# Optimization experiments

Hardware: AMD Instinct MI355X
Metric: run time of the kernel (lower is better)

Reference implementation:

```python
import jax, jax.numpy as jnp
import numpy as np

DIM = 2048
N_HEADS = 16
Q_LORA = 1536
KV_LORA = 512
NOPE = 128
ROPE = 64
V_DIM = 128
B, T = 1, 3072
EPS = 1e-6


def rmsnorm(x, w):
    var = jnp.mean(jnp.square(x), axis=-1, keepdims=True)
    return x * jax.lax.rsqrt(var + EPS) * w


def apply_rope(x, cos, sin):
    # x: (B, T, H, d); cos/sin: (T, d//2) -> broadcast (1, T, 1, d//2)
    c = cos[None, :, None, :]
    s = sin[None, :, None, :]
    x1 = x[..., 0::2]
    x2 = x[..., 1::2]
    r1 = x1 * c - x2 * s
    r2 = x1 * s + x2 * c
    return jnp.stack([r1, r2], axis=-1).reshape(x.shape)


def setup_inputs() -> dict:
    key = jax.random.key(0)
    ks = jax.random.split(key, 10)
    std = 0.02
    x = jax.random.normal(ks[0], (B, T, DIM), dtype=jnp.float32)
    # RoPE angles: position * inv_freq, shape (T, ROPE//2)
    inv_freq = 1.0 / (10000.0 ** (np.arange(0, ROPE, 2, dtype=np.float32) / ROPE))
    freqs = jnp.asarray(np.arange(T, dtype=np.float32)[:, None] * inv_freq[None, :])
    # additive causal mask (T, T)
    mask = jnp.where(jnp.tril(jnp.ones((T, T), dtype=bool)), 0.0, -jnp.inf).astype(jnp.float32)
    wq_down = jax.random.normal(ks[1], (DIM, Q_LORA), dtype=jnp.float32) * std
    q_norm_w = jnp.ones((Q_LORA,), dtype=jnp.float32)
    wq_nope = jax.random.normal(ks[2], (Q_LORA, N_HEADS * NOPE), dtype=jnp.float32) * std
    wq_rope = jax.random.normal(ks[3], (Q_LORA, N_HEADS * ROPE), dtype=jnp.float32) * std
    wkv_down = jax.random.normal(ks[4], (DIM, KV_LORA + ROPE), dtype=jnp.float32) * std
    kv_norm_w = jnp.ones((KV_LORA,), dtype=jnp.float32)
    wkv_up = jax.random.normal(ks[5], (KV_LORA, N_HEADS * (NOPE + V_DIM)), dtype=jnp.float32) * std
    wo = jax.random.normal(ks[6], (N_HEADS * V_DIM, DIM), dtype=jnp.float32) * std
    return {
        'x': x, 'freqs': freqs, 'mask': mask,
        'wq_down': wq_down, 'q_norm_w': q_norm_w, 'wq_nope': wq_nope,
        'wq_rope': wq_rope, 'wkv_down': wkv_down, 'kv_norm_w': kv_norm_w,
        'wkv_up': wkv_up, 'wo': wo,
    }


def reference(x, freqs, mask, wq_down, q_norm_w, wq_nope, wq_rope,
              wkv_down, kv_norm_w, wkv_up, wo):
    cos, sin = jnp.cos(freqs), jnp.sin(freqs)
    # Q path: down-project, RMSNorm, split nope/rope heads
    q_lat = rmsnorm(x @ wq_down, q_norm_w)                      # (B,T,Q_LORA)
    q_nope = (q_lat @ wq_nope).reshape(B, T, N_HEADS, NOPE)
    q_rope = apply_rope((q_lat @ wq_rope).reshape(B, T, N_HEADS, ROPE), cos, sin)
    q = jnp.concatenate([q_nope, q_rope], axis=-1)              # (B,T,H,192)
    # KV path: joint down-projection -> latent c_kv + raw rope key
    kvd = x @ wkv_down                                          # (B,T,KV_LORA+ROPE)
    c_kv = kvd[..., :KV_LORA]
    k_rope_raw = kvd[..., KV_LORA:]                             # (B,T,ROPE)
    k_rope = jnp.broadcast_to(k_rope_raw[:, :, None, :], (B, T, N_HEADS, ROPE))
    k_rope = apply_rope(k_rope, cos, sin)
    kv_up = (rmsnorm(c_kv, kv_norm_w) @ wkv_up).reshape(B, T, N_HEADS, NOPE + V_DIM)
    k_nope = kv_up[..., :NOPE]
    v = kv_up[..., NOPE:]                                       # (B,T,H,V_DIM)
    k = jnp.concatenate([k_nope, k_rope], axis=-1)              # (B,T,H,192)
    scale = (NOPE + ROPE) ** (-0.5)
    attn = jnp.einsum('bqhd,bkhd->bhqk', q, k) * scale + mask[None, None]
    attn = jax.nn.softmax(attn, axis=-1)                        # dropout p=0 (eval)
    out = jnp.einsum('bhqk,bkhd->bqhd', attn, v).reshape(B, T, N_HEADS * V_DIM)
    return out @ wo                                             # (B,T,DIM)
```

## Files before the change

### kernel.cpp

```cpp
#include <hip/hip_runtime.h>
#include <hip/hip_bf16.h>

typedef __bf16 bf16_t;
typedef __bf16 bf16x8 __attribute__((ext_vector_type(8)));
typedef float f32x4 __attribute__((ext_vector_type(4)));

#define T_SEQ 3072
#define DIM 2048
#define NH 16
#define QLORA 1536
#define KVLORA 512
#define NOPE 128
#define ROPE 64
#define VDIM 128
#define HD 192
#define SCALE 0.07216878364870323f
#define CHUNK 12

#define T1KV_LD 2112
#define QNR_LD 3072

__device__ inline float wave_reduce_sum(float v) {
    #pragma unroll
    for (int off = 32; off > 0; off >>= 1) v += __shfl_down(v, off);
    return v;
}

__device__ inline float block_reduce_sum_256(float v) {
    __shared__ float red[4];
    int lane = threadIdx.x & 63, w = threadIdx.x >> 6;
    v = wave_reduce_sum(v);
    if (lane == 0) red[w] = v;
    __syncthreads();
    if (threadIdx.x == 0) red[0] = red[0] + red[1] + red[2] + red[3];
    __syncthreads();
    return red[0];
}

__device__ inline void glds16(const bf16_t* g, bf16_t* l) {
    __builtin_amdgcn_global_load_lds(
        (const __attribute__((address_space(1))) unsigned int*)g,
        (__attribute__((address_space(3))) unsigned int*)l, 16, 0, 0);
}

__global__ void f2b_kernel(const float* __restrict__ in, bf16_t* __restrict__ out, int n) {
    int i = (blockIdx.x * 256 + threadIdx.x) * 4;
    if (i < n) {
        float4 v = *(const float4*)&in[i];
        bf16_t o[4] = {(bf16_t)v.x, (bf16_t)v.y, (bf16_t)v.z, (bf16_t)v.w};
        *(uint2*)&out[i] = *(const uint2*)o;
    }
}

__global__ __launch_bounds__(256) void transp_kernel(
    const float* __restrict__ in, bf16_t* __restrict__ out, int K, int N)
{
    __shared__ float tile[32][33];
    int k0 = blockIdx.y * 32, n0 = blockIdx.x * 32;
    int tx = threadIdx.x & 31, ty = threadIdx.x >> 5;
    #pragma unroll
    for (int i = 0; i < 4; ++i)
        tile[ty + i * 8][tx] = in[(size_t)(k0 + ty + i * 8) * N + n0 + tx];
    __syncthreads();
    #pragma unroll
    for (int i = 0; i < 4; ++i)
        out[(size_t)(n0 + ty + i * 8) * K + k0 + tx] = (bf16_t)tile[tx][ty + i * 8];
}

__global__ __launch_bounds__(256) void vt_transp(
    const bf16_t* __restrict__ kvu, bf16_t* __restrict__ vt)
{
    __shared__ bf16_t tile[32][34];
    int t0 = blockIdx.x * 32, d0 = blockIdx.y * 32, h = blockIdx.z;
    int tx = threadIdx.x & 31, ty = threadIdx.x >> 5;
    #pragma unroll
    for (int i = 0; i < 4; ++i)
        tile[ty + i * 8][tx] = kvu[(size_t)(t0 + ty + i * 8) * (NH * 256) + h * 256 + NOPE + d0 + tx];
    __syncthreads();
    #pragma unroll
    for (int i = 0; i < 4; ++i)
        vt[((size_t)h * VDIM + d0 + ty + i * 8) * T_SEQ + t0 + tx] = tile[tx][ty + i * 8];
}

__global__ __launch_bounds__(256) void gemm_mfma(
    const bf16_t* __restrict__ A, const bf16_t* __restrict__ Bt,
    float* __restrict__ Cf, bf16_t* __restrict__ Cb,
    int M, int N, int K, int lda, int ldb, int ldc, int writef)
{
    __shared__ __align__(16) bf16_t As[2][128 * 32];
    __shared__ __align__(16) bf16_t Bs[2][128 * 32];
    int tid = threadIdx.x;
    int w = tid >> 6, lane = tid & 63;
    int quad = lane >> 4, l16 = lane & 15;
    int bm = blockIdx.y * 128, bn = blockIdx.x * 128;
    int wm = (w & 1) * 64, wn = (w >> 1) * 64;

    int srow = tid >> 2, soff = (tid & 3) * 8;
    const bf16_t* a0 = A + (size_t)(bm + srow) * lda + soff;
    const bf16_t* a1 = A + (size_t)(bm + 64 + srow) * lda + soff;
    int br0 = bn + srow;      if (br0 >= N) br0 = N - 1;
    int br1 = bn + 64 + srow; if (br1 >= N) br1 = N - 1;
    const bf16_t* b0 = Bt + (size_t)br0 * ldb + soff;
    const bf16_t* b1 = Bt + (size_t)br1 * ldb + soff;

    f32x4 acc[4][4];
    #pragma unroll
    for (int i = 0; i < 4; ++i)
        #pragma unroll
        for (int j = 0; j < 4; ++j)
            acc[i][j] = (f32x4){0.f, 0.f, 0.f, 0.f};

    int nk = K >> 5;
    glds16(a0, &As[0][tid * 8]);
    glds16(a1, &As[0][tid * 8 + 2048]);
    glds16(b0, &Bs[0][tid * 8]);
    glds16(b1, &Bs[0][tid * 8 + 2048]);
    a0 += 32; a1 += 32; b0 += 32; b1 += 32;

    for (int t = 0; t < nk; ++t) {
        int cur = t & 1;
        if (t + 1 < nk) {
            int nxt = cur ^ 1;
            glds16(a0, &As[nxt][tid * 8]);
            glds16(a1, &As[nxt][tid * 8 + 2048]);
            glds16(b0, &Bs[nxt][tid * 8]);
            glds16(b1, &Bs[nxt][tid * 8 + 2048]);
            a0 += 32; a1 += 32; b0 += 32; b1 += 32;
            asm volatile("s_waitcnt vmcnt(4)" ::: "memory");
        } else {
            asm volatile("s_waitcnt vmcnt(0)" ::: "memory");
        }
        __builtin_amdgcn_s_barrier();
        __builtin_amdgcn_sched_barrier(0);

        bf16x8 af[4], bfr[4];
        #pragma unroll
        for (int t4 = 0; t4 < 4; ++t4) {
            af[t4]  = *(const bf16x8*)&As[cur][(wm + t4 * 16 + l16) * 32 + quad * 8];
            bfr[t4] = *(const bf16x8*)&Bs[cur][(wn + t4 * 16 + l16) * 32 + quad * 8];
        }
        #pragma unroll
        for (int i = 0; i < 4; ++i)
            #pragma unroll
            for (int j = 0; j < 4; ++j)
                acc[i][j] = __builtin_amdgcn_mfma_f32_16x16x32_bf16(af[i], bfr[j], acc[i][j], 0, 0, 0);

        __builtin_amdgcn_sched_barrier(0);
        __builtin_amdgcn_s_barrier();
        __builtin_amdgcn_sched_barrier(0);
    }

    #pragma unroll
    for (int i = 0; i < 4; ++i) {
        #pragma unroll
        for (int j = 0; j < 4; ++j) {
            #pragma unroll
            for (int r = 0; r < 4; ++r) {
                int row = bm + wm + i * 16 + quad * 4 + r;
                int col = bn + wn + j * 16 + l16;
                if (col < N) {
                    if (writef) Cf[(size_t)row * ldc + col] = acc[i][j][r];
                    else        Cb[(size_t)row * ldc + col] = (bf16_t)acc[i][j][r];
                }
            }
        }
    }
}

__global__ __launch_bounds__(256) void rmsnorm_rows(
    bf16_t* __restrict__ X, const float* __restrict__ w, int N, int ld)
{
    int row = blockIdx.x;
    bf16_t* x = X + (size_t)row * ld;
    float ss = 0.f;
    for (int i = threadIdx.x; i < N; i += 256) { float v = (float)x[i]; ss += v * v; }
    ss = block_reduce_sum_256(ss);
    float sc = rsqrtf(ss / (float)N + 1e-6f);
    for (int i = threadIdx.x; i < N; i += 256)
        x[i] = (bf16_t)((float)x[i] * sc * w[i]);
}

__global__ __launch_bounds__(256) void kv_post(
    const bf16_t* __restrict__ kvd, const float* __restrict__ w,
    const float* __restrict__ freqs,
    bf16_t* __restrict__ ckvn, bf16_t* __restrict__ kr)
{
    int row = blockIdx.x;
    const bf16_t* src = kvd + (size_t)row * T1KV_LD;
    float ss = 0.f;
    for (int i = threadIdx.x; i < KVLORA; i += 256) { float v = (float)src[i]; ss += v * v; }
    ss = block_reduce_sum_256(ss);
    float sc = rsqrtf(ss / (float)KVLORA + 1e-6f);
    for (int i = threadIdx.x; i < KVLORA; i += 256)
        ckvn[(size_t)row * KVLORA + i] = (bf16_t)((float)src[i] * sc * w[i]);
    if (threadIdx.x < 32) {
        int i = threadIdx.x;
        float f = freqs[row * 32 + i];
        float c = cosf(f), s = sinf(f);
        float x1 = (float)src[KVLORA + 2 * i], x2 = (float)src[KVLORA + 2 * i + 1];
        kr[(size_t)row * ROPE + 2 * i]     = (bf16_t)(x1 * c - x2 * s);
        kr[(size_t)row * ROPE + 2 * i + 1] = (bf16_t)(x1 * s + x2 * c);
    }
}

__global__ void rope_q(bf16_t* __restrict__ qr, const float* __restrict__ freqs) {
    int idx = blockIdx.x * 256 + threadIdx.x;
    if (idx >= T_SEQ * NH * 32) return;
    int t = idx >> 9;
    int rem = idx & 511;
    int h = rem >> 5;
    int i = rem & 31;
    float f = freqs[t * 32 + i];
    float c = cosf(f), s = sinf(f);
    bf16_t* p = qr + (size_t)t * QNR_LD + h * ROPE + 2 * i;
    float x1 = (float)p[0], x2 = (float)p[1];
    p[0] = (bf16_t)(x1 * c - x2 * s);
    p[1] = (bf16_t)(x1 * s + x2 * c);
}

#define P_STRIDE 72
__device__ inline int slot_base(int qt, int h) {
    int b = qt / CHUNK;
    return h * 120 + qt + 6 * b * (b - 1) + (qt - CHUNK * b) * b;
}
__global__ __launch_bounds__(256) void attn_v12(
    const bf16_t* __restrict__ QNR,
    const bf16_t* __restrict__ KVU, const bf16_t* __restrict__ KR,
    const bf16_t* __restrict__ Vt,
    bf16_t* __restrict__ Opart, float* __restrict__ lpart)
{
    __shared__ __align__(16) bf16_t Kn[64 * 128];
    __shared__ __align__(16) bf16_t Kr[64 * 64];
    __shared__ __align__(16) bf16_t Vs[128 * 64];
    __shared__ __align__(16) bf16_t Ps[4][16 * P_STRIDE];

    int qt = (T_SEQ / 64 - 1) - blockIdx.x;
    int cx = blockIdx.y, h = blockIdx.z;
    if (cx > qt / CHUNK) return;
    int slot = slot_base(qt, h) + cx;
    int kt0 = cx * CHUNK;
    int kt1 = min(qt + 1, kt0 + CHUNK);

    int tid = threadIdx.x;
    int w = tid >> 6, lane = tid & 63;
    int quad = lane >> 4, l16 = lane & 15;
    int qbase = qt * 64;

    bf16x8 qf[6];
    {
        int qrow = qbase + w * 16 + l16;
        #pragma unroll
        for (int kk = 0; kk < 4; ++kk)
            qf[kk] = *(const bf16x8*)&QNR[(size_t)qrow * QNR_LD + h * NOPE + kk * 32 + quad * 8];
        #pragma unroll
        for (int kk = 4; kk < 6; ++kk)
            qf[kk] = *(const bf16x8*)&QNR[(size_t)qrow * QNR_LD + (NH * NOPE) + h * ROPE + (kk - 4) * 32 + quad * 8];
    }

    int l4 = lane >> 4, l3 = lane >> 3;
    const bf16_t* kn_e = KVU + (size_t)(kt0 * 64 + w * 16 + l4) * (NH * 256) + h * 256 + ((lane & 15) ^ l4) * 8;
    const bf16_t* kn_o = KVU + (size_t)(kt0 * 64 + w * 16 + l4) * (NH * 256) + h * 256 + ((lane & 15) ^ (4 + l4)) * 8;
    const bf16_t* krp  = KR  + (size_t)(kt0 * 64 + w * 16 + l3) * ROPE + ((lane & 7) ^ l3) * 8;
    const bf16_t* vp   = Vt  + ((size_t)h * VDIM + w * 32 + l3) * T_SEQ + kt0 * 64 + ((lane & 7) ^ l3) * 8;

    bf16x8 ones;
    #pragma unroll
    for (int i = 0; i < 8; ++i) ones[i] = (bf16_t)1.0f;

    f32x4 o[8];
    #pragma unroll
    for (int nt = 0; nt < 8; ++nt) o[nt] = (f32x4){0.f, 0.f, 0.f, 0.f};
    f32x4 lacc = (f32x4){0.f, 0.f, 0.f, 0.f};

    for (int kt = kt0; kt < kt1; ++kt) {
        int kbase = kt * 64;
        #pragma unroll
        for (int i = 0; i < 4; ++i)
            glds16(((i & 1) ? kn_o : kn_e) + (size_t)i * 4 * (NH * 256), &Kn[(w * 4 + i) * 512]);
        #pragma unroll
        for (int i = 0; i < 2; ++i)
            glds16(krp + (size_t)i * 8 * ROPE, &Kr[(w * 2 + i) * 512]);
        #pragma unroll
        for (int i = 0; i < 4; ++i)
            glds16(vp + (size_t)i * 8 * T_SEQ, &Vs[(w * 4 + i) * 512]);
        kn_e += (size_t)64 * NH * 256;
        kn_o += (size_t)64 * NH * 256;
        krp  += 64 * ROPE;
        vp   += 64;
        __syncthreads();

        f32x4 S[4];
        #pragma unroll
        for (int c = 0; c < 4; ++c) S[c] = (f32x4){0.f, 0.f, 0.f, 0.f};
        #pragma unroll
        for (int kk = 0; kk < 4; ++kk) {
            #pragma unroll
            for (int c = 0; c < 4; ++c) {
                bf16x8 kf = *(const bf16x8*)&Kn[(c * 16 + l16) * 128 + (((kk * 4 + quad) ^ (l16 & 7)) * 8)];
                S[c] = __builtin_amdgcn_mfma_f32_16x16x32_bf16(qf[kk], kf, S[c], 0, 0, 0);
            }
        }
        #pragma unroll
        for (int kk = 4; kk < 6; ++kk) {
            #pragma unroll
            for (int c = 0; c < 4; ++c) {
                bf16x8 kf = *(const bf16x8*)&Kr[(c * 16 + l16) * 64 + ((((kk - 4) * 4 + quad) ^ (l16 & 7)) * 8)];
                S[c] = __builtin_amdgcn_mfma_f32_16x16x32_bf16(qf[kk], kf, S[c], 0, 0, 0);
            }
        }

        #pragma unroll
        for (int c = 0; c < 4; ++c) {
            #pragma unroll
            for (int j = 0; j < 4; ++j) {
                int col = kbase + c * 16 + l16;
                int grow = qbase + w * 16 + quad * 4 + j;
                float p = (col <= grow) ? __expf(S[c][j] * SCALE) : 0.f;
                Ps[w][(quad * 4 + j) * P_STRIDE + c * 16 + l16] = (bf16_t)p;
            }
        }
        __asm__ volatile("s_waitcnt lgkmcnt(0)" ::: "memory");

        bf16x8 pf0 = *(const bf16x8*)&Ps[w][l16 * P_STRIDE + quad * 8];
        bf16x8 pf1 = *(const bf16x8*)&Ps[w][l16 * P_STRIDE + 32 + quad * 8];
        lacc = __builtin_amdgcn_mfma_f32_16x16x32_bf16(pf0, ones, lacc, 0, 0, 0);
        lacc = __builtin_amdgcn_mfma_f32_16x16x32_bf16(pf1, ones, lacc, 0, 0, 0);

        #pragma unroll
        for (int kk2 = 0; kk2 < 2; ++kk2) {
            bf16x8 pf = kk2 ? pf1 : pf0;
            #pragma unroll
            for (int nt = 0; nt < 8; ++nt) {
                bf16x8 vf = *(const bf16x8*)&Vs[(nt * 16 + l16) * 64 + (((kk2 * 4 + quad) ^ (l16 & 7)) * 8)];
                o[nt] = __builtin_amdgcn_mfma_f32_16x16x32_bf16(pf, vf, o[nt], 0, 0, 0);
            }
        }
        __syncthreads();
    }

    #pragma unroll
    for (int nt = 0; nt < 8; ++nt)
        #pragma unroll
        for (int j = 0; j < 4; ++j)
            Opart[(size_t)slot * 8192 + (w * 16 + quad * 4 + j) * 128 + nt * 16 + l16] = (bf16_t)o[nt][j];
    if (l16 == 0) {
        #pragma unroll
        for (int j = 0; j < 4; ++j)
            lpart[slot * 64 + w * 16 + quad * 4 + j] = lacc[j];
    }
}

__global__ __launch_bounds__(256) void attn_combine(
    const bf16_t* __restrict__ Opart, const float* __restrict__ lpart,
    bf16_t* __restrict__ AO)
{
    int qt = blockIdx.x, h = blockIdx.y;
    int nch = qt / CHUNK + 1;
    int base = slot_base(qt, h);
    int r = threadIdx.x >> 2, c0 = (threadIdx.x & 3) * 32;

    float acc[32];
    #pragma unroll
    for (int i = 0; i < 32; ++i) acc[i] = 0.f;
    float lsum = 0.f;
    for (int ch = 0; ch < nch; ++ch) {
        int slot = base + ch;
        const bf16_t* p = &Opart[(size_t)slot * 8192 + r * 128 + c0];
        #pragma unroll
        for (int v = 0; v < 4; ++v) {
            bf16x8 u = *(const bf16x8*)&p[v * 8];
            #pragma unroll
            for (int e = 0; e < 8; ++e) acc[v * 8 + e] += (float)u[e];
        }
        lsum += lpart[slot * 64 + r];
    }
    float inv = 1.0f / lsum;
    bf16_t* dst = AO + (size_t)(qt * 64 + r) * (NH * VDIM) + h * VDIM + c0;
    #pragma unroll
    for (int v = 0; v < 4; ++v) {
        bf16_t tmp[8];
        #pragma unroll
        for (int e = 0; e < 8; ++e) tmp[e] = (bf16_t)(acc[v * 8 + e] * inv);
        *(uint4*)&dst[v * 8] = *(const uint4*)tmp;
    }
}

extern "C" void kernel_launch(void* const* d_in, const int* in_sizes, int n_in,
                              void* d_out, int out_size, void* d_ws, size_t ws_size,
                              hipStream_t stream) {
    const float* x        = (const float*)d_in[0];
    const float* freqs    = (const float*)d_in[1];
    const float* wq_down  = (const float*)d_in[3];
    const float* q_norm_w = (const float*)d_in[4];
    const float* wq_nope  = (const float*)d_in[5];
    const float* wq_rope  = (const float*)d_in[6];
    const float* wkv_down = (const float*)d_in[7];
    const float* kv_norm_w= (const float*)d_in[8];
    const float* wkv_up   = (const float*)d_in[9];
    const float* wo       = (const float*)d_in[10];
    float* out = (float*)d_out;

    bf16_t* ws = (bf16_t*)d_ws;
    bf16_t* xb     = ws;
    bf16_t* wqd_t  = xb     + 6291456;
    bf16_t* wkvd_t = wqd_t  + 3145728;
    bf16_t* wqn_t  = wkvd_t + 1179648;
    bf16_t* wqr_t  = wqn_t  + 3145728;
    bf16_t* wkvu_t = wqr_t  + 1572864;
    bf16_t* t1kv   = wkvu_t + 2097152;
    bf16_t* ckvn   = t1kv   + 6488064;
    bf16_t* Opart  = ws;
    float*  lpart  = (float*)(ws + 15728640);
    bf16_t* ao     = ws + 15728640 + 245760;
    bf16_t* wo_t   = ws    + 25493504;
    bf16_t* kr     = wo_t  + 4194304;
    bf16_t* qnr    = kr    + 196608;
    bf16_t* kvu    = qnr   + 9437184;
    bf16_t* vt     = kvu   + 12582912;

    f2b_kernel<<<T_SEQ * DIM / 4 / 256, 256, 0, stream>>>(x, xb, T_SEQ * DIM);
    transp_kernel<<<dim3(QLORA / 32, DIM / 32), 256, 0, stream>>>(wq_down, wqd_t, DIM, QLORA);
    transp_kernel<<<dim3((KVLORA + ROPE) / 32, DIM / 32), 256, 0, stream>>>(wkv_down, wkvd_t, DIM, KVLORA + ROPE);
    transp_kernel<<<dim3(NH * NOPE / 32, QLORA / 32), 256, 0, stream>>>(wq_nope, wqn_t, QLORA, NH * NOPE);
    transp_kernel<<<dim3(NH * ROPE / 32, QLORA / 32), 256, 0, stream>>>(wq_rope, wqr_t, QLORA, NH * ROPE);
    transp_kernel<<<dim3(NH * 256 / 32, KVLORA / 32), 256, 0, stream>>>(wkv_up, wkvu_t, KVLORA, NH * 256);
    transp_kernel<<<dim3(DIM / 32, DIM / 32), 256, 0, stream>>>(wo, wo_t, DIM, DIM);

    gemm_mfma<<<dim3(17, T_SEQ / 128), 256, 0, stream>>>(
        xb, wqd_t, nullptr, t1kv, T_SEQ, 2112, DIM, DIM, DIM, T1KV_LD, 0);

    rmsnorm_rows<<<T_SEQ, 256, 0, stream>>>(t1kv, q_norm_w, QLORA, T1KV_LD);
    kv_post<<<T_SEQ, 256, 0, stream>>>(t1kv + QLORA, kv_norm_w, freqs, ckvn, kr);

    gemm_mfma<<<dim3(24, T_SEQ / 128), 256, 0, stream>>>(
        t1kv, wqn_t, nullptr, qnr, T_SEQ, 3072, QLORA, T1KV_LD, QLORA, QNR_LD, 0);
    rope_q<<<(T_SEQ * NH * 32 + 255) / 256, 256, 0, stream>>>(qnr + NH * NOPE, freqs);

    gemm_mfma<<<dim3(NH * 256 / 128, T_SEQ / 128), 256, 0, stream>>>(
        ckvn, wkvu_t, nullptr, kvu, T_SEQ, NH * 256, KVLORA, KVLORA, KVLORA, NH * 256, 0);

    vt_transp<<<dim3(T_SEQ / 32, VDIM / 32, NH), 256, 0, stream>>>(kvu, vt);

    attn_v12<<<dim3(T_SEQ / 64, 4, NH), 256, 0, stream>>>(qnr, kvu, kr, vt, Opart, lpart);
    attn_combine<<<dim3(T_SEQ / 64, NH), 256, 0, stream>>>(Opart, lpart, ao);

    gemm_mfma<<<dim3(DIM / 128, T_SEQ / 128), 256, 0, stream>>>(
        ao, wo_t, out, nullptr, T_SEQ, DIM, DIM, DIM, DIM, DIM, 1);
}
```

Before: 475.0 us.

## Pair short and long causal query tiles per block for balanced attention work

```diff
diff --git a/kernel.cpp b/kernel.cpp
--- a/kernel.cpp
+++ b/kernel.cpp
@@ -15,7 +15,6 @@
 #define VDIM 128
 #define HD 192
 #define SCALE 0.07216878364870323f
-#define CHUNK 12
 
 #define T1KV_LD 2112
 #define QNR_LD 3072
@@ -219,28 +218,13 @@
 }
 
 #define P_STRIDE 72
-__device__ inline int slot_base(int qt, int h) {
-    int b = qt / CHUNK;
-    return h * 120 + qt + 6 * b * (b - 1) + (qt - CHUNK * b) * b;
-}
-__global__ __launch_bounds__(256) void attn_v12(
-    const bf16_t* __restrict__ QNR,
-    const bf16_t* __restrict__ KVU, const bf16_t* __restrict__ KR,
-    const bf16_t* __restrict__ Vt,
-    bf16_t* __restrict__ Opart, float* __restrict__ lpart)
-{
-    __shared__ __align__(16) bf16_t Kn[64 * 128];
-    __shared__ __align__(16) bf16_t Kr[64 * 64];
-    __shared__ __align__(16) bf16_t Vs[128 * 64];
-    __shared__ __align__(16) bf16_t Ps[4][16 * P_STRIDE];
-
-    int qt = (T_SEQ / 64 - 1) - blockIdx.x;
-    int cx = blockIdx.y, h = blockIdx.z;
-    if (cx > qt / CHUNK) return;
-    int slot = slot_base(qt, h) + cx;
-    int kt0 = cx * CHUNK;
-    int kt1 = min(qt + 1, kt0 + CHUNK);
-
+__device__ __forceinline__ void flash_range(
+    const bf16_t* __restrict__ QNR, const bf16_t* __restrict__ KVU,
+    const bf16_t* __restrict__ KR, const bf16_t* __restrict__ Vt,
+    bf16_t* Kn, bf16_t* Kr, bf16_t* Vs, bf16_t* Ps,
+    int h, int qt, int kt0, int kt1,
+    f32x4 o[8], f32x4& lacc)
+{
     int tid = threadIdx.x;
     int w = tid >> 6, lane = tid & 63;
     int quad = lane >> 4, l16 = lane & 15;
@@ -266,11 +250,6 @@
     bf16x8 ones;
     #pragma unroll
     for (int i = 0; i < 8; ++i) ones[i] = (bf16_t)1.0f;
-
-    f32x4 o[8];
-    #pragma unroll
-    for (int nt = 0; nt < 8; ++nt) o[nt] = (f32x4){0.f, 0.f, 0.f, 0.f};
-    f32x4 lacc = (f32x4){0.f, 0.f, 0.f, 0.f};
 
     for (int kt = kt0; kt < kt1; ++kt) {
         int kbase = kt * 64;
@@ -316,13 +295,13 @@
                 int col = kbase + c * 16 + l16;
                 int grow = qbase + w * 16 + quad * 4 + j;
                 float p = (col <= grow) ? __expf(S[c][j] * SCALE) : 0.f;
-                Ps[w][(quad * 4 + j) * P_STRIDE + c * 16 + l16] = (bf16_t)p;
+                Ps[(quad * 4 + j) * P_STRIDE + c * 16 + l16] = (bf16_t)p;
             }
         }
         __asm__ volatile("s_waitcnt lgkmcnt(0)" ::: "memory");
 
-        bf16x8 pf0 = *(const bf16x8*)&Ps[w][l16 * P_STRIDE + quad * 8];
-        bf16x8 pf1 = *(const bf16x8*)&Ps[w][l16 * P_STRIDE + 32 + quad * 8];
+        bf16x8 pf0 = *(const bf16x8*)&Ps[l16 * P_STRIDE + quad * 8];
+        bf16x8 pf1 = *(const bf16x8*)&Ps[l16 * P_STRIDE + 32 + quad * 8];
         lacc = __builtin_amdgcn_mfma_f32_16x16x32_bf16(pf0, ones, lacc, 0, 0, 0);
         lacc = __builtin_amdgcn_mfma_f32_16x16x32_bf16(pf1, ones, lacc, 0, 0, 0);
 
@@ -337,16 +316,73 @@
         }
         __syncthreads();
     }
-
-    #pragma unroll
-    for (int nt = 0; nt < 8; ++nt)
-        #pragma unroll
-        for (int j = 0; j < 4; ++j)
-            Opart[(size_t)slot * 8192 + (w * 16 + quad * 4 + j) * 128 + nt * 16 + l16] = (bf16_t)o[nt][j];
-    if (l16 == 0) {
-        #pragma unroll
-        for (int j = 0; j < 4; ++j)
-            lpart[slot * 64 + w * 16 + quad * 4 + j] = lacc[j];
+}
+
+__global__ __launch_bounds__(256) void attn_v13(
+    const bf16_t* __restrict__ QNR,
+    const bf16_t* __restrict__ KVU, const bf16_t* __restrict__ KR,
+    const bf16_t* __restrict__ Vt,
+    bf16_t* __restrict__ AO, bf16_t* __restrict__ Opart, float* __restrict__ lpart)
+{
+    __shared__ __align__(16) bf16_t Kn[64 * 128];
+    __shared__ __align__(16) bf16_t Kr[64 * 64];
+    __shared__ __align__(16) bf16_t Vs[128 * 64];
+    __shared__ __align__(16) bf16_t Ps[4][16 * P_STRIDE];
+
+    int half = blockIdx.x, p = blockIdx.y, h = blockIdx.z;
+    int b = 47 - p;
+    int tid = threadIdx.x;
+    int w = tid >> 6, lane = tid & 63;
+    int quad = lane >> 4, l16 = lane & 15;
+    bf16_t* ps = Ps[w];
+
+    f32x4 o[8];
+    f32x4 lacc;
+
+    if (half == 0) {
+        #pragma unroll
+        for (int nt = 0; nt < 8; ++nt) o[nt] = (f32x4){0.f, 0.f, 0.f, 0.f};
+        lacc = (f32x4){0.f, 0.f, 0.f, 0.f};
+        flash_range(QNR, KVU, KR, Vt, Kn, Kr, Vs, ps, h, p, 0, p + 1, o, lacc);
+        #pragma unroll
+        for (int j = 0; j < 4; ++j) {
+            float inv = 1.0f / lacc[j];
+            int row = p * 64 + w * 16 + quad * 4 + j;
+            #pragma unroll
+            for (int nt = 0; nt < 8; ++nt)
+                AO[(size_t)row * (NH * VDIM) + h * VDIM + nt * 16 + l16] = (bf16_t)(o[nt][j] * inv);
+        }
+        #pragma unroll
+        for (int nt = 0; nt < 8; ++nt) o[nt] = (f32x4){0.f, 0.f, 0.f, 0.f};
+        lacc = (f32x4){0.f, 0.f, 0.f, 0.f};
+        flash_range(QNR, KVU, KR, Vt, Kn, Kr, Vs, ps, h, b, 0, 24 - p, o, lacc);
+        int slot = (h * 24 + (23 - p)) * 2 + 0;
+        #pragma unroll
+        for (int nt = 0; nt < 8; ++nt)
+            #pragma unroll
+            for (int j = 0; j < 4; ++j)
+                Opart[(size_t)slot * 8192 + (w * 16 + quad * 4 + j) * 128 + nt * 16 + l16] = (bf16_t)o[nt][j];
+        if (l16 == 0) {
+            #pragma unroll
+            for (int j = 0; j < 4; ++j)
+                lpart[slot * 64 + w * 16 + quad * 4 + j] = lacc[j];
+        }
+    } else {
+        #pragma unroll
+        for (int nt = 0; nt < 8; ++nt) o[nt] = (f32x4){0.f, 0.f, 0.f, 0.f};
+        lacc = (f32x4){0.f, 0.f, 0.f, 0.f};
+        flash_range(QNR, KVU, KR, Vt, Kn, Kr, Vs, ps, h, b, 24 - p, b + 1, o, lacc);
+        int slot = (h * 24 + (23 - p)) * 2 + 1;
+        #pragma unroll
+        for (int nt = 0; nt < 8; ++nt)
+            #pragma unroll
+            for (int j = 0; j < 4; ++j)
+                Opart[(size_t)slot * 8192 + (w * 16 + quad * 4 + j) * 128 + nt * 16 + l16] = (bf16_t)o[nt][j];
+        if (l16 == 0) {
+            #pragma unroll
+            for (int j = 0; j < 4; ++j)
+                lpart[slot * 64 + w * 16 + quad * 4 + j] = lacc[j];
+        }
     }
 }
 
@@ -354,28 +390,28 @@
     const bf16_t* __restrict__ Opart, const float* __restrict__ lpart,
     bf16_t* __restrict__ AO)
 {
-    int qt = blockIdx.x, h = blockIdx.y;
-    int nch = qt / CHUNK + 1;
-    int base = slot_base(qt, h);
+    int bt = blockIdx.x, h = blockIdx.y;
+    int base = (h * 24 + bt) * 2;
     int r = threadIdx.x >> 2, c0 = (threadIdx.x & 3) * 32;
 
     float acc[32];
     #pragma unroll
     for (int i = 0; i < 32; ++i) acc[i] = 0.f;
     float lsum = 0.f;
-    for (int ch = 0; ch < nch; ++ch) {
+    #pragma unroll
+    for (int ch = 0; ch < 2; ++ch) {
         int slot = base + ch;
-        const bf16_t* p = &Opart[(size_t)slot * 8192 + r * 128 + c0];
+        const bf16_t* pp = &Opart[(size_t)slot * 8192 + r * 128 + c0];
         #pragma unroll
         for (int v = 0; v < 4; ++v) {
-            bf16x8 u = *(const bf16x8*)&p[v * 8];
+            bf16x8 u = *(const bf16x8*)&pp[v * 8];
             #pragma unroll
             for (int e = 0; e < 8; ++e) acc[v * 8 + e] += (float)u[e];
         }
         lsum += lpart[slot * 64 + r];
     }
     float inv = 1.0f / lsum;
-    bf16_t* dst = AO + (size_t)(qt * 64 + r) * (NH * VDIM) + h * VDIM + c0;
+    bf16_t* dst = AO + (size_t)((24 + bt) * 64 + r) * (NH * VDIM) + h * VDIM + c0;
     #pragma unroll
     for (int v = 0; v < 4; ++v) {
         bf16_t tmp[8];
@@ -410,8 +446,8 @@
     bf16_t* t1kv   = wkvu_t + 2097152;
     bf16_t* ckvn   = t1kv   + 6488064;
     bf16_t* Opart  = ws;
-    float*  lpart  = (float*)(ws + 15728640);
-    bf16_t* ao     = ws + 15728640 + 245760;
+    float*  lpart  = (float*)(ws + 6291456);
+    bf16_t* ao     = ws + 6291456 + 98304;
     bf16_t* wo_t   = ws    + 25493504;
     bf16_t* kr     = wo_t  + 4194304;
     bf16_t* qnr    = kr    + 196608;
@@ -441,8 +477,8 @@
 
     vt_transp<<<dim3(T_SEQ / 32, VDIM / 32, NH), 256, 0, stream>>>(kvu, vt);
 
-    attn_v12<<<dim3(T_SEQ / 64, 4, NH), 256, 0, stream>>>(qnr, kvu, kr, vt, Opart, lpart);
-    attn_combine<<<dim3(T_SEQ / 64, NH), 256, 0, stream>>>(Opart, lpart, ao);
+    attn_v13<<<dim3(2, 24, NH), 256, 0, stream>>>(qnr, kvu, kr, vt, ao, Opart, lpart);
+    attn_combine<<<dim3(24, NH), 256, 0, stream>>>(Opart, lpart, ao);
 
     gemm_mfma<<<dim3(DIM / 128, T_SEQ / 128), 256, 0, stream>>>(
         ao, wo_t, out, nullptr, T_SEQ, DIM, DIM, DIM, DIM, DIM, 1);
```

Measured after the change: 478.6 us. Within noise of the previous version (+0.8%).
